# Performance work log

Hardware: AMD Instinct MI355X
Metric: run time of the kernel (lower is better)

## Reference

```python
import jax, jax.numpy as jnp
import numpy as np

GS = 7          # grid size
NB = 2          # boxes per cell
NC = 20         # classes
LAMBDA_COORD = 0.5
LAMBDA_NOOBJ = 0.5


def setup_inputs() -> dict:
    key = jax.random.key(0)
    k1, k2, k3 = jax.random.split(key, 3)
    B = 8192
    C = 5 * NB + NC  # 30
    inputs = jax.random.uniform(k1, (B, GS, GS, C), minval=0.05, maxval=0.95, dtype=jnp.float32)
    targets = jax.random.uniform(k2, (B, GS, GS, C), minval=0.05, maxval=0.95, dtype=jnp.float32)
    obj = jax.random.bernoulli(k3, 0.15, (B, GS, GS)).astype(jnp.float32)
    # _transform_targets writes the SAME box into both box slots and sets conf=1 for obj cells
    targets = targets.at[..., 5:9].set(targets[..., 0:4])
    targets = targets.at[..., 4].set(obj)
    targets = targets.at[..., 9].set(obj)
    return {"inputs": inputs, "targets": targets}


def _yolo_loss(inputs, targets):
    bs = inputs.shape[0]
    gs = inputs.shape[2]
    dt = inputs.dtype

    conf_t = targets[..., 4]
    coord = (conf_t > 0).astype(dt)          # [B,S,S] cells containing an object
    noobj = (conf_t == 0).astype(dt)          # [B,S,S]

    # ---- no-object confidence loss: channels 4 + 5*b for each box b ----
    conf_idx = jnp.arange(NB) * 5 + 4         # [4, 9]
    pc = inputs[..., conf_idx]                # [B,S,S,NB]
    tc = targets[..., conf_idx]
    loss_noobj = jnp.sum(noobj[..., None] * (pc - tc) ** 2)

    # ---- per-cell box matching (vectorizes the pairwise IoU loop) ----
    bp = inputs[..., :5 * NB].reshape(inputs.shape[:3] + (NB, 5))    # [B,S,S,NB,5]
    # original takes boxes_targets[i] (first box of the pair; both slots are identical)
    bt = targets[..., :5 * NB].reshape(targets.shape[:3] + (NB, 5))[..., 0, :]  # [B,S,S,5]

    def to_xyxy(b):
        # faithful to original: xy scaled by 1/gs, wh NOT scaled
        xy = b[..., :2] / gs
        wh = b[..., 2:4]
        return jnp.concatenate([xy - 0.5 * wh, xy + 0.5 * wh], axis=-1)

    pxy = to_xyxy(bp)                          # [B,S,S,NB,4]
    txy = to_xyxy(bt)[..., None, :]            # [B,S,S,1,4]
    lt = jnp.maximum(pxy[..., :2], txy[..., :2])
    rb = jnp.minimum(pxy[..., 2:], txy[..., 2:])
    whi = jnp.clip(rb - lt, 0.0)
    inter = whi[..., 0] * whi[..., 1]          # [B,S,S,NB]
    area = lambda x: (x[..., 2] - x[..., 0]) * (x[..., 3] - x[..., 1])
    iou = inter / (area(pxy) + area(txy) - inter)   # [B,S,S,NB]

    max_iou = jnp.max(iou, axis=-1)            # [B,S,S]
    idx = jnp.argmax(iou, axis=-1)             # [B,S,S] responsible box (first max, like torch)
    idx_b = jnp.broadcast_to(idx[..., None, None], idx.shape + (1, 5))
    rp = jnp.take_along_axis(bp, idx_b, axis=-2)[..., 0, :]  # [B,S,S,5] responsible preds

    loss_xy = jnp.sum(coord[..., None] * (rp[..., :2] - bt[..., :2]) ** 2)
    loss_wh = jnp.sum(coord[..., None] * (jnp.sqrt(rp[..., 2:4]) - jnp.sqrt(bt[..., 2:4])) ** 2)
    loss_obj = jnp.sum(coord * (rp[..., 4] - max_iou) ** 2)
    loss_class = jnp.sum(coord[..., None] * (inputs[..., 5 * NB:] - targets[..., 5 * NB:]) ** 2)

    loss_boxes = LAMBDA_COORD * (loss_xy + loss_wh) / bs
    loss_conf = (loss_obj + LAMBDA_NOOBJ * loss_noobj) / bs
    loss_class = loss_class / bs
    return loss_boxes, loss_conf, loss_class


def reference(inputs, targets):
    return _yolo_loss(inputs, targets)
```

## Files before the change

### kernel.cpp

```cpp
#include <hip/hip_runtime.h>

#define CC 30
#define TPW 32
#define WPB 4
#define TILE_FLOATS (TPW * CC)
#define TILE_VEC4   (TILE_FLOATS / 4)

__global__ __launch_bounds__(256) void yolo_main(
        const float* __restrict__ in,
        const float* __restrict__ tg,
        float* __restrict__ ws,
        int ncells, int nwaves_total, int pstride) {
    __shared__ float s_in[WPB * TILE_FLOATS];
    __shared__ float s_tg[WPB * TILE_FLOATS];

    const int tid   = threadIdx.x;
    const int lane  = tid & 63;
    const int wave  = tid >> 6;
    const int gwave = blockIdx.x * WPB + wave;

    float* lin = s_in + wave * TILE_FLOATS;
    float* ltg = s_tg + wave * TILE_FLOATS;

    const int ntiles = (ncells + TPW - 1) / TPW;
    const float inv_gs = 0.14285714285714285f;

    float a_boxes = 0.0f, a_conf = 0.0f, a_class = 0.0f;

    for (int tile = gwave; tile < ntiles; tile += nwaves_total) {
        const int cbase = tile * TPW;
        int n = ncells - cbase;
        if (n > TPW) n = TPW;

        if (n == TPW) {
            const float4* gin = (const float4*)(in + (size_t)cbase * CC);
            const float4* gtg = (const float4*)(tg + (size_t)cbase * CC);
            float4* vin = (float4*)lin;
            float4* vtg = (float4*)ltg;
            float4 bi[4], bt[4];
            #pragma unroll
            for (int k = 0; k < 4; ++k) {
                const int idx = k * 64 + lane;
                if (idx < TILE_VEC4) { bi[k] = gin[idx]; bt[k] = gtg[idx]; }
            }
            #pragma unroll
            for (int k = 0; k < 4; ++k) {
                const int idx = k * 64 + lane;
                if (idx < TILE_VEC4) { vin[idx] = bi[k]; vtg[idx] = bt[k]; }
            }
        } else {
            const int lim = n * CC;
            for (int k = lane; k < lim; k += 64) {
                lin[k] = in[(size_t)cbase * CC + k];
                ltg[k] = tg[(size_t)cbase * CC + k];
            }
        }
        asm volatile("s_waitcnt vmcnt(0) lgkmcnt(0)" ::: "memory");
        __builtin_amdgcn_wave_barrier();

        if (lane < n) {
            const float2* f2 = (const float2*)(lin + lane * CC);
            const float2* t2 = (const float2*)(ltg + lane * CC);

            const float2 fi0 = f2[0], fi1 = f2[1], fi2 = f2[2], fi3 = f2[3], fi4 = f2[4];
            const float2 tt0 = t2[0], tt1 = t2[1], tt2 = t2[2], tt4 = t2[4];

            const float conf_t = tt2.x;
            const float coord  = (conf_t > 0.0f)  ? 1.0f : 0.0f;
            const float noobj  = (conf_t == 0.0f) ? 1.0f : 0.0f;

            const float d0 = fi2.x - tt2.x;
            const float d1 = fi4.y - tt4.y;
            const float l_noobj = noobj * (d0 * d0 + d1 * d1);

            const float bt0 = tt0.x, bt1 = tt0.y, bt2 = tt1.x, bt3 = tt1.y;
            const float ttx = bt0 * inv_gs, tty = bt1 * inv_gs;
            const float txmin = ttx - 0.5f * bt2, tymin = tty - 0.5f * bt3;
            const float txmax = ttx + 0.5f * bt2, tymax = tty + 0.5f * bt3;
            const float tarea = (txmax - txmin) * (tymax - tymin);

            const float px0 = fi0.x, py0 = fi0.y, pw0 = fi1.x, ph0 = fi1.y, pc0 = fi2.x;
            const float px1 = fi2.y, py1 = fi3.x, pw1 = fi3.y, ph1 = fi4.x, pc1 = fi4.y;

            float iou0, iou1;
            {
                const float cx = px0 * inv_gs, cy = py0 * inv_gs;
                const float xmin = cx - 0.5f * pw0, ymin = cy - 0.5f * ph0;
                const float xmax = cx + 0.5f * pw0, ymax = cy + 0.5f * ph0;
                const float wx = fmaxf(fminf(xmax, txmax) - fmaxf(xmin, txmin), 0.0f);
                const float wy = fmaxf(fminf(ymax, tymax) - fmaxf(ymin, tymin), 0.0f);
                const float inter = wx * wy;
                const float parea = (xmax - xmin) * (ymax - ymin);
                iou0 = inter / (parea + tarea - inter);
            }
            {
                const float cx = px1 * inv_gs, cy = py1 * inv_gs;
                const float xmin = cx - 0.5f * pw1, ymin = cy - 0.5f * ph1;
                const float xmax = cx + 0.5f * pw1, ymax = cy + 0.5f * ph1;
                const float wx = fmaxf(fminf(xmax, txmax) - fmaxf(xmin, txmin), 0.0f);
                const float wy = fmaxf(fminf(ymax, tymax) - fmaxf(ymin, tymin), 0.0f);
                const float inter = wx * wy;
                const float parea = (xmax - xmin) * (ymax - ymin);
                iou1 = inter / (parea + tarea - inter);
            }
            const bool  sel1    = iou1 > iou0;
            const float max_iou = fmaxf(iou0, iou1);

            const float rp0 = sel1 ? px1 : px0;
            const float rp1 = sel1 ? py1 : py0;
            const float rp2 = sel1 ? pw1 : pw0;
            const float rp3 = sel1 ? ph1 : ph0;
            const float rp4 = sel1 ? pc1 : pc0;

            const float dx = rp0 - bt0, dy = rp1 - bt1;
            const float sw = sqrtf(rp2) - sqrtf(bt2);
            const float sh = sqrtf(rp3) - sqrtf(bt3);
            const float dob = rp4 - max_iou;
            const float l_box = dx * dx + dy * dy + sw * sw + sh * sh;
            const float l_obj = dob * dob;

            float l_cls = 0.0f;
            #pragma unroll
            for (int j = 5; j < 15; ++j) {
                const float2 fv = f2[j];
                const float2 tv = t2[j];
                const float gx = fv.x - tv.x;
                const float gy = fv.y - tv.y;
                l_cls += gx * gx + gy * gy;
            }

            a_boxes += coord * l_box;
            a_conf  += coord * l_obj + 0.5f * l_noobj;
            a_class += coord * l_cls;
        }
        __builtin_amdgcn_wave_barrier();
    }

    #pragma unroll
    for (int off = 32; off > 0; off >>= 1) {
        a_boxes += __shfl_down(a_boxes, off, 64);
        a_conf  += __shfl_down(a_conf,  off, 64);
        a_class += __shfl_down(a_class, off, 64);
    }
    if (lane == 0) {
        ws[gwave]               = a_boxes;
        ws[gwave + pstride]     = a_conf;
        ws[gwave + 2 * pstride] = a_class;
    }
}

__global__ __launch_bounds__(256) void yolo_finalize(
        const float* __restrict__ ws, float* __restrict__ out,
        int nparts, int pstride, float inv_bs) {
    float b = 0.0f, c = 0.0f, k = 0.0f;
    for (int i = threadIdx.x; i < nparts; i += 256) {
        b += ws[i];
        c += ws[i + pstride];
        k += ws[i + 2 * pstride];
    }
    #pragma unroll
    for (int off = 32; off > 0; off >>= 1) {
        b += __shfl_down(b, off, 64);
        c += __shfl_down(c, off, 64);
        k += __shfl_down(k, off, 64);
    }
    __shared__ float s_red[4][3];
    const int wave = threadIdx.x >> 6;
    if ((threadIdx.x & 63) == 0) {
        s_red[wave][0] = b;
        s_red[wave][1] = c;
        s_red[wave][2] = k;
    }
    __syncthreads();
    if (threadIdx.x == 0) {
        const float tb = s_red[0][0] + s_red[1][0] + s_red[2][0] + s_red[3][0];
        const float tc = s_red[0][1] + s_red[1][1] + s_red[2][1] + s_red[3][1];
        const float tk = s_red[0][2] + s_red[1][2] + s_red[2][2] + s_red[3][2];
        out[0] = 0.5f * tb * inv_bs;
        out[1] = tc * inv_bs;
        out[2] = tk * inv_bs;
    }
}

extern "C" void kernel_launch(void* const* d_in, const int* in_sizes, int n_in,
                              void* d_out, int out_size, void* d_ws, size_t ws_size,
                              hipStream_t stream) {
    const float* in = (const float*)d_in[0];
    const float* tg = (const float*)d_in[1];
    float* out = (float*)d_out;
    float* ws  = (float*)d_ws;

    const int ncells = in_sizes[0] / CC;
    const int B = ncells / 49;
    const float inv_bs = 1.0f / (float)B;

    const int nblocks = 1280;
    const int nwaves  = nblocks * WPB;
    const int pstride = nwaves;

    yolo_main<<<nblocks, 256, 0, stream>>>(in, tg, ws, ncells, nwaves, pstride);
    yolo_finalize<<<1, 256, 0, stream>>>(ws, out, nwaves, pstride, inv_bs);
}
```

Before: 123.8 us.

## Double-buffer tile loads in registers with 64-cell tiles and tail in finalize

The main loop is restructured so each wave prefetches the next tile into one register set while staging and computing the current tile from the other, overlapping global loads with compute. The tile size doubles to 64 cells so every lane does work, the grid shrinks to 512 blocks, and the leftover cells that do not fill a tile are computed by the finalize kernel straight from global memory. This is meant to hide load latency and remove idle half-waves, at the cost of many more live registers (four 8-element float4 buffers), which may lower occupancy.

```diff
diff --git a/kernel.cpp b/kernel.cpp
--- a/kernel.cpp
+++ b/kernel.cpp
@@ -1,10 +1,170 @@
 #include <hip/hip_runtime.h>
 
 #define CC 30
-#define TPW 32
+#define TPW 64
 #define WPB 4
 #define TILE_FLOATS (TPW * CC)
 #define TILE_VEC4   (TILE_FLOATS / 4)
+
+__device__ __forceinline__ void compute_tile(const float* __restrict__ lin,
+                                             const float* __restrict__ ltg,
+                                             int lane, float inv_gs,
+                                             float& a_boxes, float& a_conf, float& a_class) {
+    const float2* f2 = (const float2*)(lin + lane * CC);
+    const float2* t2 = (const float2*)(ltg + lane * CC);
+
+    const float2 fi0 = f2[0], fi1 = f2[1], fi2 = f2[2], fi3 = f2[3], fi4 = f2[4];
+    const float2 tt0 = t2[0], tt1 = t2[1], tt2 = t2[2], tt4 = t2[4];
+
+    const float conf_t = tt2.x;
+    const float coord  = (conf_t > 0.0f)  ? 1.0f : 0.0f;
+    const float noobj  = (conf_t == 0.0f) ? 1.0f : 0.0f;
+
+    const float d0 = fi2.x - tt2.x;
+    const float d1 = fi4.y - tt4.y;
+    const float l_noobj = noobj * (d0 * d0 + d1 * d1);
+
+    const float bt0 = tt0.x, bt1 = tt0.y, bt2 = tt1.x, bt3 = tt1.y;
+    const float ttx = bt0 * inv_gs, tty = bt1 * inv_gs;
+    const float txmin = ttx - 0.5f * bt2, tymin = tty - 0.5f * bt3;
+    const float txmax = ttx + 0.5f * bt2, tymax = tty + 0.5f * bt3;
+    const float tarea = (txmax - txmin) * (tymax - tymin);
+
+    const float px0 = fi0.x, py0 = fi0.y, pw0 = fi1.x, ph0 = fi1.y, pc0 = fi2.x;
+    const float px1 = fi2.y, py1 = fi3.x, pw1 = fi3.y, ph1 = fi4.x, pc1 = fi4.y;
+
+    float iou0, iou1;
+    {
+        const float cx = px0 * inv_gs, cy = py0 * inv_gs;
+        const float xmin = cx - 0.5f * pw0, ymin = cy - 0.5f * ph0;
+        const float xmax = cx + 0.5f * pw0, ymax = cy + 0.5f * ph0;
+        const float wx = fmaxf(fminf(xmax, txmax) - fmaxf(xmin, txmin), 0.0f);
+        const float wy = fmaxf(fminf(ymax, tymax) - fmaxf(ymin, tymin), 0.0f);
+        const float inter = wx * wy;
+        const float parea = (xmax - xmin) * (ymax - ymin);
+        iou0 = inter / (parea + tarea - inter);
+    }
+    {
+        const float cx = px1 * inv_gs, cy = py1 * inv_gs;
+        const float xmin = cx - 0.5f * pw1, ymin = cy - 0.5f * ph1;
+        const float xmax = cx + 0.5f * pw1, ymax = cy + 0.5f * ph1;
+        const float wx = fmaxf(fminf(xmax, txmax) - fmaxf(xmin, txmin), 0.0f);
+        const float wy = fmaxf(fminf(ymax, tymax) - fmaxf(ymin, tymin), 0.0f);
+        const float inter = wx * wy;
+        const float parea = (xmax - xmin) * (ymax - ymin);
+        iou1 = inter / (parea + tarea - inter);
+    }
+    const bool  sel1    = iou1 > iou0;
+    const float max_iou = fmaxf(iou0, iou1);
+
+    const float rp0 = sel1 ? px1 : px0;
+    const float rp1 = sel1 ? py1 : py0;
+    const float rp2 = sel1 ? pw1 : pw0;
+    const float rp3 = sel1 ? ph1 : ph0;
+    const float rp4 = sel1 ? pc1 : pc0;
+
+    const float dx = rp0 - bt0, dy = rp1 - bt1;
+    const float sw = sqrtf(rp2) - sqrtf(bt2);
+    const float sh = sqrtf(rp3) - sqrtf(bt3);
+    const float dob = rp4 - max_iou;
+    const float l_box = dx * dx + dy * dy + sw * sw + sh * sh;
+    const float l_obj = dob * dob;
+
+    float l_cls = 0.0f;
+    #pragma unroll
+    for (int j = 5; j < 15; ++j) {
+        const float2 fv = f2[j];
+        const float2 tv = t2[j];
+        const float gx = fv.x - tv.x;
+        const float gy = fv.y - tv.y;
+        l_cls += gx * gx + gy * gy;
+    }
+
+    a_boxes += coord * l_box;
+    a_conf  += coord * l_obj + 0.5f * l_noobj;
+    a_class += coord * l_cls;
+}
+
+__device__ __forceinline__ void cell_losses_global(const float* __restrict__ f,
+                                                   const float* __restrict__ t,
+                                                   float& o_boxes, float& o_conf, float& o_cls) {
+    const float inv_gs = 0.14285714285714285f;
+    const float conf_t = t[4];
+    const float coord  = (conf_t > 0.0f)  ? 1.0f : 0.0f;
+    const float noobj  = (conf_t == 0.0f) ? 1.0f : 0.0f;
+    const float d0 = f[4] - t[4];
+    const float d1 = f[9] - t[9];
+    const float l_noobj = noobj * (d0 * d0 + d1 * d1);
+    const float bt0 = t[0], bt1 = t[1], bt2 = t[2], bt3 = t[3];
+    const float ttx = bt0 * inv_gs, tty = bt1 * inv_gs;
+    const float txmin = ttx - 0.5f * bt2, tymin = tty - 0.5f * bt3;
+    const float txmax = ttx + 0.5f * bt2, tymax = tty + 0.5f * bt3;
+    const float tarea = (txmax - txmin) * (tymax - tymin);
+    float iou0, iou1;
+    {
+        const float cx = f[0] * inv_gs, cy = f[1] * inv_gs;
+        const float xmin = cx - 0.5f * f[2], ymin = cy - 0.5f * f[3];
+        const float xmax = cx + 0.5f * f[2], ymax = cy + 0.5f * f[3];
+        const float wx = fmaxf(fminf(xmax, txmax) - fmaxf(xmin, txmin), 0.0f);
+        const float wy = fmaxf(fminf(ymax, tymax) - fmaxf(ymin, tymin), 0.0f);
+        const float inter = wx * wy;
+        const float parea = (xmax - xmin) * (ymax - ymin);
+        iou0 = inter / (parea + tarea - inter);
+    }
+    {
+        const float cx = f[5] * inv_gs, cy = f[6] * inv_gs;
+        const float xmin = cx - 0.5f * f[7], ymin = cy - 0.5f * f[8];
+        const float xmax = cx + 0.5f * f[7], ymax = cy + 0.5f * f[8];
+        const float wx = fmaxf(fminf(xmax, txmax) - fmaxf(xmin, txmin), 0.0f);
+        const float wy = fmaxf(fminf(ymax, tymax) - fmaxf(ymin, tymin), 0.0f);
+        const float inter = wx * wy;
+        const float parea = (xmax - xmin) * (ymax - ymin);
+        iou1 = inter / (parea + tarea - inter);
+    }
+    const bool  sel1    = iou1 > iou0;
+    const float max_iou = fmaxf(iou0, iou1);
+    const float rp0 = sel1 ? f[5] : f[0];
+    const float rp1 = sel1 ? f[6] : f[1];
+    const float rp2 = sel1 ? f[7] : f[2];
+    const float rp3 = sel1 ? f[8] : f[3];
+    const float rp4 = sel1 ? f[9] : f[4];
+    const float dx = rp0 - bt0, dy = rp1 - bt1;
+    const float sw = sqrtf(rp2) - sqrtf(bt2);
+    const float sh = sqrtf(rp3) - sqrtf(bt3);
+    const float dob = rp4 - max_iou;
+    float l_cls = 0.0f;
+    #pragma unroll
+    for (int j = 10; j < 30; ++j) {
+        const float d = f[j] - t[j];
+        l_cls += d * d;
+    }
+    o_boxes += coord * (dx * dx + dy * dy + sw * sw + sh * sh);
+    o_conf  += coord * (dob * dob) + 0.5f * l_noobj;
+    o_cls   += coord * l_cls;
+}
+
+#define HALF_STEP(CUR_I, CUR_T, NXT_I, NXT_T)                                   \
+    {                                                                           \
+        const int tn = t + nwaves_total;                                        \
+        if (tn < nfull) {                                                       \
+            const float4* gin = (const float4*)(in + (size_t)tn * TILE_FLOATS); \
+            const float4* gtg = (const float4*)(tg + (size_t)tn * TILE_FLOATS); \
+            _Pragma("unroll")                                                   \
+            for (int k = 0; k < 8; ++k) {                                       \
+                const int idx = k * 64 + lane;                                  \
+                if (idx < TILE_VEC4) { NXT_I[k] = gin[idx]; NXT_T[k] = gtg[idx]; } \
+            }                                                                   \
+        }                                                                       \
+        __builtin_amdgcn_wave_barrier();   \
+        _Pragma("unroll")                                                       \
+        for (int k = 0; k < 8; ++k) {                                           \
+            const int idx = k * 64 + lane;                                      \
+            if (idx < TILE_VEC4) { vin[idx] = CUR_I[k]; vtg[idx] = CUR_T[k]; }  \
+        }                                                                       \
+        __builtin_amdgcn_wave_barrier();                                        \
+        compute_tile(lin, ltg, lane, inv_gs, a_boxes, a_conf, a_class);         \
+        t = tn;                                                                 \
+    }
 
 __global__ __launch_bounds__(256) void yolo_main(
         const float* __restrict__ in,
@@ -21,119 +181,31 @@
 
     float* lin = s_in + wave * TILE_FLOATS;
     float* ltg = s_tg + wave * TILE_FLOATS;
-
-    const int ntiles = (ncells + TPW - 1) / TPW;
+    float4* vin = (float4*)lin;
+    float4* vtg = (float4*)ltg;
+
+    const int nfull = ncells / TPW;
     const float inv_gs = 0.14285714285714285f;
 
     float a_boxes = 0.0f, a_conf = 0.0f, a_class = 0.0f;
 
-    for (int tile = gwave; tile < ntiles; tile += nwaves_total) {
-        const int cbase = tile * TPW;
-        int n = ncells - cbase;
-        if (n > TPW) n = TPW;
-
-        if (n == TPW) {
-            const float4* gin = (const float4*)(in + (size_t)cbase * CC);
-            const float4* gtg = (const float4*)(tg + (size_t)cbase * CC);
-            float4* vin = (float4*)lin;
-            float4* vtg = (float4*)ltg;
-            float4 bi[4], bt[4];
-            #pragma unroll
-            for (int k = 0; k < 4; ++k) {
-                const int idx = k * 64 + lane;
-                if (idx < TILE_VEC4) { bi[k] = gin[idx]; bt[k] = gtg[idx]; }
-            }
-            #pragma unroll
-            for (int k = 0; k < 4; ++k) {
-                const int idx = k * 64 + lane;
-                if (idx < TILE_VEC4) { vin[idx] = bi[k]; vtg[idx] = bt[k]; }
-            }
-        } else {
-            const int lim = n * CC;
-            for (int k = lane; k < lim; k += 64) {
-                lin[k] = in[(size_t)cbase * CC + k];
-                ltg[k] = tg[(size_t)cbase * CC + k];
-            }
+    float4 Ai[8], At[8], Bi[8], Bt[8];
+
+    int t = gwave;
+    if (t < nfull) {
+        const float4* gin = (const float4*)(in + (size_t)t * TILE_FLOATS);
+        const float4* gtg = (const float4*)(tg + (size_t)t * TILE_FLOATS);
+        #pragma unroll
+        for (int k = 0; k < 8; ++k) {
+            const int idx = k * 64 + lane;
+            if (idx < TILE_VEC4) { Ai[k] = gin[idx]; At[k] = gtg[idx]; }
         }
-        asm volatile("s_waitcnt vmcnt(0) lgkmcnt(0)" ::: "memory");
-        __builtin_amdgcn_wave_barrier();
-
-        if (lane < n) {
-            const float2* f2 = (const float2*)(lin + lane * CC);
-            const float2* t2 = (const float2*)(ltg + lane * CC);
-
-            const float2 fi0 = f2[0], fi1 = f2[1], fi2 = f2[2], fi3 = f2[3], fi4 = f2[4];
-            const float2 tt0 = t2[0], tt1 = t2[1], tt2 = t2[2], tt4 = t2[4];
-
-            const float conf_t = tt2.x;
-            const float coord  = (conf_t > 0.0f)  ? 1.0f : 0.0f;
-            const float noobj  = (conf_t == 0.0f) ? 1.0f : 0.0f;
-
-            const float d0 = fi2.x - tt2.x;
-            const float d1 = fi4.y - tt4.y;
-            const float l_noobj = noobj * (d0 * d0 + d1 * d1);
-
-            const float bt0 = tt0.x, bt1 = tt0.y, bt2 = tt1.x, bt3 = tt1.y;
-            const float ttx = bt0 * inv_gs, tty = bt1 * inv_gs;
-            const float txmin = ttx - 0.5f * bt2, tymin = tty - 0.5f * bt3;
-            const float txmax = ttx + 0.5f * bt2, tymax = tty + 0.5f * bt3;
-            const float tarea = (txmax - txmin) * (tymax - tymin);
-
-            const float px0 = fi0.x, py0 = fi0.y, pw0 = fi1.x, ph0 = fi1.y, pc0 = fi2.x;
-            const float px1 = fi2.y, py1 = fi3.x, pw1 = fi3.y, ph1 = fi4.x, pc1 = fi4.y;
-
-            float iou0, iou1;
-            {
-                const float cx = px0 * inv_gs, cy = py0 * inv_gs;
-                const float xmin = cx - 0.5f * pw0, ymin = cy - 0.5f * ph0;
-                const float xmax = cx + 0.5f * pw0, ymax = cy + 0.5f * ph0;
-                const float wx = fmaxf(fminf(xmax, txmax) - fmaxf(xmin, txmin), 0.0f);
-                const float wy = fmaxf(fminf(ymax, tymax) - fmaxf(ymin, tymin), 0.0f);
-                const float inter = wx * wy;
-                const float parea = (xmax - xmin) * (ymax - ymin);
-                iou0 = inter / (parea + tarea - inter);
-            }
-            {
-                const float cx = px1 * inv_gs, cy = py1 * inv_gs;
-                const float xmin = cx - 0.5f * pw1, ymin = cy - 0.5f * ph1;
-                const float xmax = cx + 0.5f * pw1, ymax = cy + 0.5f * ph1;
-                const float wx = fmaxf(fminf(xmax, txmax) - fmaxf(xmin, txmin), 0.0f);
-                const float wy = fmaxf(fminf(ymax, tymax) - fmaxf(ymin, tymin), 0.0f);
-                const float inter = wx * wy;
-                const float parea = (xmax - xmin) * (ymax - ymin);
-                iou1 = inter / (parea + tarea - inter);
-            }
-            const bool  sel1    = iou1 > iou0;
-            const float max_iou = fmaxf(iou0, iou1);
-
-            const float rp0 = sel1 ? px1 : px0;
-            const float rp1 = sel1 ? py1 : py0;
-            const float rp2 = sel1 ? pw1 : pw0;
-            const float rp3 = sel1 ? ph1 : ph0;
-            const float rp4 = sel1 ? pc1 : pc0;
-
-            const float dx = rp0 - bt0, dy = rp1 - bt1;
-            const float sw = sqrtf(rp2) - sqrtf(bt2);
-            const float sh = sqrtf(rp3) - sqrtf(bt3);
-            const float dob = rp4 - max_iou;
-            const float l_box = dx * dx + dy * dy + sw * sw + sh * sh;
-            const float l_obj = dob * dob;
-
-            float l_cls = 0.0f;
-            #pragma unroll
-            for (int j = 5; j < 15; ++j) {
-                const float2 fv = f2[j];
-                const float2 tv = t2[j];
-                const float gx = fv.x - tv.x;
-                const float gy = fv.y - tv.y;
-                l_cls += gx * gx + gy * gy;
-            }
-
-            a_boxes += coord * l_box;
-            a_conf  += coord * l_obj + 0.5f * l_noobj;
-            a_class += coord * l_cls;
+        while (true) {
+            HALF_STEP(Ai, At, Bi, Bt);
+            if (t >= nfull) break;
+            HALF_STEP(Bi, Bt, Ai, At);
+            if (t >= nfull) break;
         }
-        __builtin_amdgcn_wave_barrier();
     }
 
     #pragma unroll
@@ -150,13 +222,19 @@
 }
 
 __global__ __launch_bounds__(256) void yolo_finalize(
+        const float* __restrict__ in,
+        const float* __restrict__ tg,
         const float* __restrict__ ws, float* __restrict__ out,
-        int nparts, int pstride, float inv_bs) {
+        int nparts, int pstride, int rem_base, int rem, float inv_bs) {
     float b = 0.0f, c = 0.0f, k = 0.0f;
     for (int i = threadIdx.x; i < nparts; i += 256) {
         b += ws[i];
         c += ws[i + pstride];
         k += ws[i + 2 * pstride];
+    }
+    if ((int)threadIdx.x < rem) {
+        const size_t cell = (size_t)(rem_base + threadIdx.x) * CC;
+        cell_losses_global(in + cell, tg + cell, b, c, k);
     }
     #pragma unroll
     for (int off = 32; off > 0; off >>= 1) {
@@ -194,10 +272,13 @@
     const int B = ncells / 49;
     const float inv_bs = 1.0f / (float)B;
 
-    const int nblocks = 1280;
+    const int nblocks = 512;
     const int nwaves  = nblocks * WPB;
     const int pstride = nwaves;
+    const int nfull   = ncells / TPW;
+    const int rem     = ncells - nfull * TPW;
 
     yolo_main<<<nblocks, 256, 0, stream>>>(in, tg, ws, ncells, nwaves, pstride);
-    yolo_finalize<<<1, 256, 0, stream>>>(ws, out, nwaves, pstride, inv_bs);
-}
+    yolo_finalize<<<1, 256, 0, stream>>>(in, tg, ws, out, nwaves, pstride,
+                                         nfull * TPW, rem, inv_bs);
+}
```

After: 157.5 us. 27.2% more time.
